# Kernel tuning notes

Hardware: AMD Instinct MI355X
Metric: run time of the kernel (lower is better)

## Reference

```python
import jax, jax.numpy as jnp
import numpy as np

GAMMA = 1.7015043497085571  # variance-preserving gelu gain (fnn nonlinearity)
FOV_DEG = 37.5              # retina angular scale per isotropic grid unit
EPS = 1e-6

N, C, H_IN, W_IN = 256, 3, 270, 480
F_EYE, FEAT = 2, 32
H_OUT, W_OUT = 144, 256


def _iso_grid(h, w):
    # isotropic pixel-center grid: shorter side spans ~[-1, 1]
    s = min(h, w)
    y = ((jnp.arange(h, dtype=jnp.float32) + 0.5) * 2.0 - h) / s
    x = ((jnp.arange(w, dtype=jnp.float32) + 0.5) * 2.0 - w) / s
    gx, gy = jnp.meshgrid(x, y, indexing="xy")  # each [h, w]
    return gx, gy


def _rmat_3d(ax, ay, az):
    # rotation = Rz @ Ry @ Rx, batched over leading dim
    o = jnp.zeros_like(ax); i = jnp.ones_like(ax)
    cx, sx = jnp.cos(ax), jnp.sin(ax)
    cy, sy = jnp.cos(ay), jnp.sin(ay)
    cz, sz = jnp.cos(az), jnp.sin(az)
    Rx = jnp.stack([i, o, o, o, cx, -sx, o, sx, cx], -1).reshape(-1, 3, 3)
    Ry = jnp.stack([cy, o, sy, o, i, o, -sy, o, cy], -1).reshape(-1, 3, 3)
    Rz = jnp.stack([cz, -sz, o, sz, cz, o, o, o, i], -1).reshape(-1, 3, 3)
    return Rz @ Ry @ Rx


def _isotropic_grid_sample_2d(img, grid, pad_value=0.0):
    # img: [n, c, h, w]; grid: [n, h', w', 2] isotropic coords (short side -> [-1,1])
    # bilinear, align_corners=False, constant padding via a 1-px pad ring + clamp
    n, c, h, w = img.shape
    s = min(h, w)
    fx = (grid[..., 0] * (s / w) + 1.0) * w / 2.0 - 0.5 + 1.0  # +1 for pad ring
    fy = (grid[..., 1] * (s / h) + 1.0) * h / 2.0 - 0.5 + 1.0
    imgp = jnp.pad(img, ((0, 0), (0, 0), (1, 1), (1, 1)), constant_values=pad_value)
    imgp = imgp.transpose(0, 2, 3, 1)  # [n, h+2, w+2, c]
    x0 = jnp.floor(fx); y0 = jnp.floor(fy)
    wx = (fx - x0)[..., None]; wy = (fy - y0)[..., None]
    x0i = jnp.clip(x0.astype(jnp.int32), 0, w + 1)
    x1i = jnp.clip(x0.astype(jnp.int32) + 1, 0, w + 1)
    y0i = jnp.clip(y0.astype(jnp.int32), 0, h + 1)
    y1i = jnp.clip(y0.astype(jnp.int32) + 1, 0, h + 1)
    b = jnp.arange(n)[:, None, None]
    v00 = imgp[b, y0i, x0i]; v01 = imgp[b, y0i, x1i]
    v10 = imgp[b, y1i, x0i]; v11 = imgp[b, y1i, x1i]
    out = (v00 * (1 - wx) * (1 - wy) + v01 * wx * (1 - wy)
           + v10 * (1 - wx) * wy + v11 * wx * wy)
    return out.transpose(0, 3, 1, 2)  # [n, c, h', w']


def setup_inputs() -> dict:
    key = jax.random.key(0)
    ks = jax.random.split(key, 5)
    return {
        "stimulus": jax.random.normal(ks[0], (N, C, H_IN, W_IN), jnp.float32),
        "eye_position": jax.random.normal(ks[1], (N, F_EYE), jnp.float32),
        "W0": jax.random.normal(ks[2], (F_EYE, FEAT), jnp.float32) * 0.3,
        "b0": jnp.zeros((FEAT,), jnp.float32),
        "W1": jax.random.normal(ks[3], (FEAT, FEAT), jnp.float32) * 0.15,
        "b1": jnp.zeros((FEAT,), jnp.float32),
        "Wp": jax.random.normal(ks[4], (FEAT, 3), jnp.float32) * 0.05,
        "bp": jnp.zeros((3,), jnp.float32),
        "height": H_OUT,
        "width": W_OUT,
    }


def reference(stimulus, eye_position, W0, b0, W1, b1, Wp, bp, height, width):
    # tiny per-sample MLP -> 3 rotation angles (fnn rmat path)
    x = jax.nn.gelu(eye_position @ W0 + b0) * GAMMA
    x = jax.nn.gelu(x @ W1 + b1) * GAMMA
    ang = x @ Wp + bp                                   # [n, 3]
    R = _rmat_3d(ang[:, 0], ang[:, 1], ang[:, 2])       # [n, 3, 3]

    # retina rays: angular grid -> unit directions, rotated by R
    gx, gy = _iso_grid(height, width)                   # [h', w']
    r = jnp.sqrt(gx * gx + gy * gy)
    theta = r * jnp.float32(np.deg2rad(FOV_DEG))
    safe_r = jnp.maximum(r, EPS)
    sin_t = jnp.sin(theta)
    d = jnp.stack([sin_t * gx / safe_r, sin_t * gy / safe_r, jnp.cos(theta)], -1)
    rays = jnp.einsum("nij,hwj->nhwi", R, d)            # [n, h', w', 3]

    # monitor plane projection at distance 1 along +z
    z = jnp.maximum(rays[..., 2], EPS)
    grid = jnp.stack([rays[..., 0] / z, rays[..., 1] / z], -1)  # [n, h', w', 2]

    return _isotropic_grid_sample_2d(stimulus, grid, 0.0)
```

## Files before the change

kernel.cpp:

```cpp
#include <hip/hip_runtime.h>
#include <math.h>

#define N_S   256
#define C_IN  3
#define H_IN  270
#define W_IN  480
#define H_OUT 144
#define W_OUT 256
#define FEAT  32
#define HW_IN  (H_IN * W_IN)
#define HW_OUT (H_OUT * W_OUT)

#define GAMMA_F 1.7015043497085571f
#define FOV_RAD 0.6544984694978736f
#define SQRT_2_OVER_PI 0.7978845608028654f

#define WS_R_OFF  0
#define WS_D_OFF  16384

__device__ __forceinline__ float gelu_gamma(float x) {
    float t = tanhf(SQRT_2_OVER_PI * (x + 0.044715f * x * x * x));
    return 0.5f * x * (1.0f + t) * GAMMA_F;
}

__global__ __launch_bounds__(64) void mlp_rot_kernel(
    const float* __restrict__ eye,
    const float* __restrict__ W0, const float* __restrict__ b0,
    const float* __restrict__ W1, const float* __restrict__ b1,
    const float* __restrict__ Wp, const float* __restrict__ bp,
    float* __restrict__ wsR)
{
    __shared__ float h_s[FEAT];
    __shared__ float ang_s[3];
    __shared__ float R_s[9];
    const int n   = blockIdx.x;
    const int tid = threadIdx.x;

    if (tid < FEAT) {
        const float e0 = eye[n * 2 + 0];
        const float e1 = eye[n * 2 + 1];
        float a = fmaf(e0, W0[tid], fmaf(e1, W0[FEAT + tid], b0[tid]));
        h_s[tid] = gelu_gamma(a);
    }
    __syncthreads();
    float h1v = 0.0f;
    if (tid < FEAT) {
        float acc = b1[tid];
        #pragma unroll
        for (int k = 0; k < FEAT; ++k) acc = fmaf(h_s[k], W1[k * FEAT + tid], acc);
        h1v = gelu_gamma(acc);
    }
    __syncthreads();
    if (tid < FEAT) h_s[tid] = h1v;
    __syncthreads();
    if (tid < 3) {
        float acc = bp[tid];
        #pragma unroll
        for (int k = 0; k < FEAT; ++k) acc = fmaf(h_s[k], Wp[k * 3 + tid], acc);
        ang_s[tid] = acc;
    }
    __syncthreads();
    if (tid == 0) {
        const float cx = cosf(ang_s[0]), sx = sinf(ang_s[0]);
        const float cy = cosf(ang_s[1]), sy = sinf(ang_s[1]);
        const float cz = cosf(ang_s[2]), sz = sinf(ang_s[2]);
        R_s[0] = cz * cy; R_s[1] = cz * sy * sx - sz * cx; R_s[2] = cz * sy * cx + sz * sx;
        R_s[3] = sz * cy; R_s[4] = sz * sy * sx + cz * cx; R_s[5] = sz * sy * cx - cz * sx;
        R_s[6] = -sy;     R_s[7] = cy * sx;                R_s[8] = cy * cx;
    }
    __syncthreads();
    if (tid < 9) wsR[n * 9 + tid] = R_s[tid];
}

__global__ __launch_bounds__(256) void ray_table_kernel(float4* __restrict__ wsD)
{
    const int i = blockIdx.x * 256 + threadIdx.x;
    const int h = i >> 8;
    const int w = i & 255;

    const float inv_s = 1.0f / 144.0f;
    const float gx = ((w + 0.5f) * 2.0f - (float)W_OUT) * inv_s;
    const float gy = ((h + 0.5f) * 2.0f - (float)H_OUT) * inv_s;

    const float r     = sqrtf(gx * gx + gy * gy);
    const float theta = r * FOV_RAD;
    const float sr    = fmaxf(r, 1e-6f);
    const float st    = sinf(theta);
    float4 d;
    d.x = st * gx / sr;
    d.y = st * gy / sr;
    d.z = cosf(theta);
    d.w = 0.0f;
    wsD[i] = d;
}

struct __attribute__((packed, aligned(4))) f2a { float x, y; };

__global__ __launch_bounds__(256) void retina_sample_kernel(
    const float* __restrict__ stim,
    const float* __restrict__ wsR,
    const float4* __restrict__ wsD,
    float* __restrict__ out)
{
    const int blk  = blockIdx.x;
    const int work = ((blk & 7) * (N_S * H_OUT / 8)) + (blk >> 3);
    const int n   = work / H_OUT;
    const int h   = work - n * H_OUT;
    const int tid = threadIdx.x;

    float Rm[9];
    #pragma unroll
    for (int i = 0; i < 9; ++i) Rm[i] = wsR[n * 9 + i];

    const float4 d = wsD[h * W_OUT + tid];

    const float rxv = fmaf(Rm[0], d.x, fmaf(Rm[1], d.y, Rm[2] * d.z));
    const float ryv = fmaf(Rm[3], d.x, fmaf(Rm[4], d.y, Rm[5] * d.z));
    const float rzv = fmaf(Rm[6], d.x, fmaf(Rm[7], d.y, Rm[8] * d.z));

    const float z     = fmaxf(rzv, 1e-6f);
    const float inv_z = __builtin_amdgcn_rcpf(z);
    const float px = rxv * inv_z;
    const float py = ryv * inv_z;

    float fx = fmaf(px, 135.0f, 240.5f);
    float fy = fmaf(py, 135.0f, 135.5f);
    fx = fminf(fmaxf(fx, -100.0f), 100000.0f);
    fy = fminf(fmaxf(fy, -100.0f), 100000.0f);

    const float x0f = floorf(fx), y0f = floorf(fy);
    const float wx = fx - x0f,   wy = fy - y0f;
    const int x0 = (int)x0f, y0 = (int)y0f;
    const int cx0 = x0 - 1, cx1 = x0;
    const int cy0 = y0 - 1, cy1 = y0;

    const float wxa = ((unsigned)cx0 < (unsigned)W_IN) ? (1.0f - wx) : 0.0f;
    const float wxb = ((unsigned)cx1 < (unsigned)W_IN) ? wx          : 0.0f;
    const float wya = ((unsigned)cy0 < (unsigned)H_IN) ? (1.0f - wy) : 0.0f;
    const float wyb = ((unsigned)cy1 < (unsigned)H_IN) ? wy          : 0.0f;

    const int b = min(max(cx0, 0), W_IN - 2);
    const float wl = (cx0 == b) ? wxa : ((cx0 == b - 1) ? wxb : 0.0f);
    const float wr = (cx0 == b) ? wxb : ((cx0 == b + 1) ? wxa : 0.0f);
    const int yb = min(max(cy0, 0), H_IN - 2);
    const float wt = (cy0 == yb) ? wya : ((cy0 == yb - 1) ? wyb : 0.0f);
    const float wb = (cy0 == yb) ? wyb : ((cy0 == yb + 1) ? wya : 0.0f);

    const float c00 = wt * wl, c01 = wt * wr;
    const float c10 = wb * wl, c11 = wb * wr;

    const float* __restrict__ p0 = stim + (size_t)n * (C_IN * HW_IN) + yb * W_IN + b;
    const float* __restrict__ q0 = p0 + W_IN;

    const f2a a0 = *reinterpret_cast<const f2a*>(p0);
    const f2a a1 = *reinterpret_cast<const f2a*>(q0);
    const f2a b0 = *reinterpret_cast<const f2a*>(p0 + HW_IN);
    const f2a b1 = *reinterpret_cast<const f2a*>(q0 + HW_IN);
    const f2a c0 = *reinterpret_cast<const f2a*>(p0 + 2 * HW_IN);
    const f2a c1 = *reinterpret_cast<const f2a*>(q0 + 2 * HW_IN);

    const float r0 = fmaf(a0.x, c00, fmaf(a0.y, c01, fmaf(a1.x, c10, a1.y * c11)));
    const float r1 = fmaf(b0.x, c00, fmaf(b0.y, c01, fmaf(b1.x, c10, b1.y * c11)));
    const float r2 = fmaf(c0.x, c00, fmaf(c0.y, c01, fmaf(c1.x, c10, c1.y * c11)));

    float* op = out + (size_t)n * (C_IN * HW_OUT) + h * W_OUT + tid;
    __builtin_nontemporal_store(r0, op);
    __builtin_nontemporal_store(r1, op + HW_OUT);
    __builtin_nontemporal_store(r2, op + 2 * HW_OUT);
}

extern "C" void kernel_launch(void* const* d_in, const int* in_sizes, int n_in,
                              void* d_out, int out_size, void* d_ws, size_t ws_size,
                              hipStream_t stream) {
    const float* stim = (const float*)d_in[0];
    const float* eye  = (const float*)d_in[1];
    const float* W0   = (const float*)d_in[2];
    const float* b0   = (const float*)d_in[3];
    const float* W1   = (const float*)d_in[4];
    const float* b1   = (const float*)d_in[5];
    const float* Wp   = (const float*)d_in[6];
    const float* bp   = (const float*)d_in[7];
    float* out = (float*)d_out;

    float*  wsR = (float*)((char*)d_ws + WS_R_OFF);
    float4* wsD = (float4*)((char*)d_ws + WS_D_OFF);

    mlp_rot_kernel<<<dim3(N_S), dim3(64), 0, stream>>>(eye, W0, b0, W1, b1, Wp, bp, wsR);
    ray_table_kernel<<<dim3(HW_OUT / 256), dim3(256), 0, stream>>>(wsD);
    retina_sample_kernel<<<dim3(N_S * H_OUT), dim3(256), 0, stream>>>(stim, wsR, wsD, out);
}
```

Baseline: 152.9 us.

## Fuse ray-direction computation into sampler and process two rows per block

Removes the separate ray table kernel and its float4 table lookup. Ray directions are now computed inline in the sampler using Taylor polynomials for sin(theta)/theta and cos(theta), which avoids the sqrt and division. Each block now handles two output rows, halving the grid size and sharing the rotation-matrix load and the column setup between them. The polynomial truncation may introduce small numerical differences at large radii, and there is less parallelism per launch.

New measurement: 135.2 us. 1.13x faster.

```diff
diff --git a/kernel.cpp b/kernel.cpp
--- a/kernel.cpp
+++ b/kernel.cpp
@@ -16,7 +16,6 @@
 #define SQRT_2_OVER_PI 0.7978845608028654f
 
 #define WS_R_OFF  0
-#define WS_D_OFF  16384
 
 __device__ __forceinline__ float gelu_gamma(float x) {
     float t = tanhf(SQRT_2_OVER_PI * (x + 0.044715f * x * x * x));
@@ -72,101 +71,102 @@
     if (tid < 9) wsR[n * 9 + tid] = R_s[tid];
 }
 
-__global__ __launch_bounds__(256) void ray_table_kernel(float4* __restrict__ wsD)
-{
-    const int i = blockIdx.x * 256 + threadIdx.x;
-    const int h = i >> 8;
-    const int w = i & 255;
-
-    const float inv_s = 1.0f / 144.0f;
-    const float gx = ((w + 0.5f) * 2.0f - (float)W_OUT) * inv_s;
-    const float gy = ((h + 0.5f) * 2.0f - (float)H_OUT) * inv_s;
-
-    const float r     = sqrtf(gx * gx + gy * gy);
-    const float theta = r * FOV_RAD;
-    const float sr    = fmaxf(r, 1e-6f);
-    const float st    = sinf(theta);
-    float4 d;
-    d.x = st * gx / sr;
-    d.y = st * gy / sr;
-    d.z = cosf(theta);
-    d.w = 0.0f;
-    wsD[i] = d;
-}
-
 struct __attribute__((packed, aligned(4))) f2a { float x, y; };
 
 __global__ __launch_bounds__(256) void retina_sample_kernel(
     const float* __restrict__ stim,
     const float* __restrict__ wsR,
-    const float4* __restrict__ wsD,
     float* __restrict__ out)
 {
     const int blk  = blockIdx.x;
-    const int work = ((blk & 7) * (N_S * H_OUT / 8)) + (blk >> 3);
-    const int n   = work / H_OUT;
-    const int h   = work - n * H_OUT;
+    const int work = ((blk & 7) * (18432 / 8)) + (blk >> 3);
+    const int n   = work / (H_OUT / 2);
+    const int hp  = work - n * (H_OUT / 2);
     const int tid = threadIdx.x;
 
     float Rm[9];
     #pragma unroll
     for (int i = 0; i < 9; ++i) Rm[i] = wsR[n * 9 + i];
 
-    const float4 d = wsD[h * W_OUT + tid];
+    const float gx  = ((tid + 0.5f) * 2.0f - (float)W_OUT) * (1.0f / 144.0f);
+    const float gx2 = gx * gx;
 
-    const float rxv = fmaf(Rm[0], d.x, fmaf(Rm[1], d.y, Rm[2] * d.z));
-    const float ryv = fmaf(Rm[3], d.x, fmaf(Rm[4], d.y, Rm[5] * d.z));
-    const float rzv = fmaf(Rm[6], d.x, fmaf(Rm[7], d.y, Rm[8] * d.z));
+    const float* __restrict__ sbase = stim + (size_t)n * (C_IN * HW_IN);
+    float* __restrict__ obase = out + (size_t)n * (C_IN * HW_OUT) + tid;
 
-    const float z     = fmaxf(rzv, 1e-6f);
-    const float inv_z = __builtin_amdgcn_rcpf(z);
-    const float px = rxv * inv_z;
-    const float py = ryv * inv_z;
+    #pragma unroll
+    for (int rr = 0; rr < 2; ++rr) {
+        const int   h  = 2 * hp + rr;
+        const float gy = ((h + 0.5f) * 2.0f - (float)H_OUT) * (1.0f / 144.0f);
+        const float u  = fmaf(gy, gy, gx2);
+        const float x  = u * (FOV_RAD * FOV_RAD);
 
-    float fx = fmaf(px, 135.0f, 240.5f);
-    float fy = fmaf(py, 135.0f, 135.5f);
-    fx = fminf(fmaxf(fx, -100.0f), 100000.0f);
-    fy = fminf(fmaxf(fy, -100.0f), 100000.0f);
+        const float sinp = 1.0f + x * (-1.6666667e-1f + x * (8.3333333e-3f
+                         + x * (-1.9841270e-4f + x * (2.7557319e-6f
+                         + x * (-2.5052108e-8f)))));
+        const float cosp = 1.0f + x * (-0.5f + x * (4.1666667e-2f
+                         + x * (-1.3888889e-3f + x * (2.4801587e-5f
+                         + x * (-2.7557319e-7f + x * 2.0876757e-9f)))));
 
-    const float x0f = floorf(fx), y0f = floorf(fy);
-    const float wx = fx - x0f,   wy = fy - y0f;
-    const int x0 = (int)x0f, y0 = (int)y0f;
-    const int cx0 = x0 - 1, cx1 = x0;
-    const int cy0 = y0 - 1, cy1 = y0;
+        const float S   = FOV_RAD * sinp;
+        const float dxv = S * gx;
+        const float dyv = S * gy;
+        const float dzv = cosp;
 
-    const float wxa = ((unsigned)cx0 < (unsigned)W_IN) ? (1.0f - wx) : 0.0f;
-    const float wxb = ((unsigned)cx1 < (unsigned)W_IN) ? wx          : 0.0f;
-    const float wya = ((unsigned)cy0 < (unsigned)H_IN) ? (1.0f - wy) : 0.0f;
-    const float wyb = ((unsigned)cy1 < (unsigned)H_IN) ? wy          : 0.0f;
+        const float rxv = fmaf(Rm[0], dxv, fmaf(Rm[1], dyv, Rm[2] * dzv));
+        const float ryv = fmaf(Rm[3], dxv, fmaf(Rm[4], dyv, Rm[5] * dzv));
+        const float rzv = fmaf(Rm[6], dxv, fmaf(Rm[7], dyv, Rm[8] * dzv));
 
-    const int b = min(max(cx0, 0), W_IN - 2);
-    const float wl = (cx0 == b) ? wxa : ((cx0 == b - 1) ? wxb : 0.0f);
-    const float wr = (cx0 == b) ? wxb : ((cx0 == b + 1) ? wxa : 0.0f);
-    const int yb = min(max(cy0, 0), H_IN - 2);
-    const float wt = (cy0 == yb) ? wya : ((cy0 == yb - 1) ? wyb : 0.0f);
-    const float wb = (cy0 == yb) ? wyb : ((cy0 == yb + 1) ? wya : 0.0f);
+        const float z     = fmaxf(rzv, 1e-6f);
+        const float inv_z = __builtin_amdgcn_rcpf(z);
+        const float px = rxv * inv_z;
+        const float py = ryv * inv_z;
 
-    const float c00 = wt * wl, c01 = wt * wr;
-    const float c10 = wb * wl, c11 = wb * wr;
+        float fx = fmaf(px, 135.0f, 240.5f);
+        float fy = fmaf(py, 135.0f, 135.5f);
+        fx = fminf(fmaxf(fx, -100.0f), 100000.0f);
+        fy = fminf(fmaxf(fy, -100.0f), 100000.0f);
 
-    const float* __restrict__ p0 = stim + (size_t)n * (C_IN * HW_IN) + yb * W_IN + b;
-    const float* __restrict__ q0 = p0 + W_IN;
+        const float x0f = floorf(fx), y0f = floorf(fy);
+        const float wx = fx - x0f,   wy = fy - y0f;
+        const int x0 = (int)x0f, y0 = (int)y0f;
+        const int cx0 = x0 - 1;
+        const int cy0 = y0 - 1;
 
-    const f2a a0 = *reinterpret_cast<const f2a*>(p0);
-    const f2a a1 = *reinterpret_cast<const f2a*>(q0);
-    const f2a b0 = *reinterpret_cast<const f2a*>(p0 + HW_IN);
-    const f2a b1 = *reinterpret_cast<const f2a*>(q0 + HW_IN);
-    const f2a c0 = *reinterpret_cast<const f2a*>(p0 + 2 * HW_IN);
-    const f2a c1 = *reinterpret_cast<const f2a*>(q0 + 2 * HW_IN);
+        const float wxa = ((unsigned)cx0       < (unsigned)W_IN) ? (1.0f - wx) : 0.0f;
+        const float wxb = ((unsigned)(cx0 + 1) < (unsigned)W_IN) ? wx          : 0.0f;
+        const float wya = ((unsigned)cy0       < (unsigned)H_IN) ? (1.0f - wy) : 0.0f;
+        const float wyb = ((unsigned)(cy0 + 1) < (unsigned)H_IN) ? wy          : 0.0f;
 
-    const float r0 = fmaf(a0.x, c00, fmaf(a0.y, c01, fmaf(a1.x, c10, a1.y * c11)));
-    const float r1 = fmaf(b0.x, c00, fmaf(b0.y, c01, fmaf(b1.x, c10, b1.y * c11)));
-    const float r2 = fmaf(c0.x, c00, fmaf(c0.y, c01, fmaf(c1.x, c10, c1.y * c11)));
+        const int b = min(max(cx0, 0), W_IN - 2);
+        const float wl = (cx0 == b) ? wxa : ((cx0 == b - 1) ? wxb : 0.0f);
+        const float wr = (cx0 == b) ? wxb : ((cx0 == b + 1) ? wxa : 0.0f);
+        const int yb = min(max(cy0, 0), H_IN - 2);
+        const float wt = (cy0 == yb) ? wya : ((cy0 == yb - 1) ? wyb : 0.0f);
+        const float wb = (cy0 == yb) ? wyb : ((cy0 == yb + 1) ? wya : 0.0f);
 
-    float* op = out + (size_t)n * (C_IN * HW_OUT) + h * W_OUT + tid;
-    __builtin_nontemporal_store(r0, op);
-    __builtin_nontemporal_store(r1, op + HW_OUT);
-    __builtin_nontemporal_store(r2, op + 2 * HW_OUT);
+        const float c00 = wt * wl, c01 = wt * wr;
+        const float c10 = wb * wl, c11 = wb * wr;
+
+        const float* __restrict__ p0 = sbase + yb * W_IN + b;
+        const float* __restrict__ q0 = p0 + W_IN;
+
+        const f2a a0 = *reinterpret_cast<const f2a*>(p0);
+        const f2a a1 = *reinterpret_cast<const f2a*>(q0);
+        const f2a b0 = *reinterpret_cast<const f2a*>(p0 + HW_IN);
+        const f2a b1 = *reinterpret_cast<const f2a*>(q0 + HW_IN);
+        const f2a c0 = *reinterpret_cast<const f2a*>(p0 + 2 * HW_IN);
+        const f2a c1 = *reinterpret_cast<const f2a*>(q0 + 2 * HW_IN);
+
+        const float r0 = fmaf(a0.x, c00, fmaf(a0.y, c01, fmaf(a1.x, c10, a1.y * c11)));
+        const float r1 = fmaf(b0.x, c00, fmaf(b0.y, c01, fmaf(b1.x, c10, b1.y * c11)));
+        const float r2 = fmaf(c0.x, c00, fmaf(c0.y, c01, fmaf(c1.x, c10, c1.y * c11)));
+
+        float* op = obase + h * W_OUT;
+        __builtin_nontemporal_store(r0, op);
+        __builtin_nontemporal_store(r1, op + HW_OUT);
+        __builtin_nontemporal_store(r2, op + 2 * HW_OUT);
+    }
 }
 
 extern "C" void kernel_launch(void* const* d_in, const int* in_sizes, int n_in,
@@ -182,10 +182,8 @@
     const float* bp   = (const float*)d_in[7];
     float* out = (float*)d_out;
 
-    float*  wsR = (float*)((char*)d_ws + WS_R_OFF);
-    float4* wsD = (float4*)((char*)d_ws + WS_D_OFF);
+    float* wsR = (float*)((char*)d_ws + WS_R_OFF);
 
     mlp_rot_kernel<<<dim3(N_S), dim3(64), 0, stream>>>(eye, W0, b0, W1, b1, Wp, bp, wsR);
-    ray_table_kernel<<<dim3(HW_OUT / 256), dim3(256), 0, stream>>>(wsD);
-    retina_sample_kernel<<<dim3(N_S * H_OUT), dim3(256), 0, stream>>>(stim, wsR, wsD, out);
+    retina_sample_kernel<<<dim3(N_S * H_OUT / 2), dim3(256), 0, stream>>>(stim, wsR, out);
 }
```
